# Optimization experiments

Hardware: AMD Instinct MI355X
Metric: run time of the kernel (lower is better)

## Reference

```python
import jax, jax.numpy as jnp
import numpy as np

ALPHA = 0.0  # module init alpha
BETA = 1.0   # default beta in set_target_with_data


def setup_inputs() -> dict:
    key = jax.random.key(0)
    k1, k2, k3, k4 = jax.random.split(key, 4)
    B, H, KP, N, D = 4, 16, 512, 4096, 64
    return {
        "K": jax.random.normal(k1, (B, H, KP, D), dtype=jnp.float32),
        "V": jax.random.normal(k2, (B, H, KP, D), dtype=jnp.float32),
        "xk": jax.random.normal(k3, (B, H, N, D), dtype=jnp.float32),
        "xv": jax.random.normal(k4, (B, H, N, D), dtype=jnp.float32),
    }


def reference(K, V, xk, xv):
    # set_target_with_data with dist_metric='dot', beta=1.0, beta2=None
    # dists: (B, H, k, n) = K @ xk^T
    dists = jnp.einsum('bhkd,bhnd->bhkn', K, xk)
    # softmax over the memory-slot axis (dim=-2)
    dk = jax.nn.softmax(BETA * dists, axis=-2)
    # normalize over the data axis (dim=-1)
    dkx = dk / jnp.sum(dk, axis=-1, keepdims=True)
    # weighted readout of data queries/values
    K_target = jnp.einsum('bhkn,bhnd->bhkd', dkx, xk)
    V_target = jnp.einsum('bhkn,bhnd->bhkd', dkx, xv)
    # set_target: grads used by maximize-SGD update
    gK = (1.0 - ALPHA) * (K_target - K)
    gV = (1.0 - ALPHA) * (V_target - V)
    return jnp.stack((gK, gV), axis=0)  # (2, B, H, k, d)
```

## Files before the change

### kernel.cpp

```cpp
#include <hip/hip_runtime.h>
#include <hip/hip_bf16.h>

typedef __bf16 bf16_t;
typedef __attribute__((ext_vector_type(8))) __bf16 bf16x8;
typedef __attribute__((ext_vector_type(4))) float f32x4;

#define BH 64
#define KP 512
#define NN 4096
#define DD 64
#define GSZ (BH * KP * DD)

#define MFMA16(a, b, c) __builtin_amdgcn_mfma_f32_16x16x32_bf16((a), (b), (c), 0, 0, 0)

__device__ __forceinline__ bf16x8 cvt8v(const f32x4 lo, const f32x4 hi) {
  bf16x8 r;
  r[0] = (bf16_t)lo[0]; r[1] = (bf16_t)lo[1]; r[2] = (bf16_t)lo[2]; r[3] = (bf16_t)lo[3];
  r[4] = (bf16_t)hi[0]; r[5] = (bf16_t)hi[1]; r[6] = (bf16_t)hi[2]; r[7] = (bf16_t)hi[3];
  return r;
}
__device__ __forceinline__ bf16x8 cvt8(const float* __restrict__ p) {
  return cvt8v(*(const f32x4*)p, *(const f32x4*)(p + 4));
}

__global__ __launch_bounds__(256) void hop_pass1(
    const float* __restrict__ Km, const float* __restrict__ xk,
    float* __restrict__ inv_colsum)
{
  __shared__ __align__(16) bf16_t Ks[128 * 72];

  const int tid  = threadIdx.x;
  const int wave = tid >> 6, lane = tid & 63;
  const int col  = lane & 15, quad = lane >> 4;
  const int bh = blockIdx.y;
  const int n0 = blockIdx.x * 256 + wave * 64;

  const float* Kb  = Km + (size_t)bh * KP * DD;
  const float* xkb = xk + (size_t)bh * NN * DD;

  bf16x8 bf[4][2];
  #pragma unroll
  for (int nsub = 0; nsub < 4; nsub++) {
    const float* p = xkb + (size_t)(n0 + nsub * 16 + col) * DD + quad * 8;
    bf[nsub][0] = cvt8(p);
    bf[nsub][1] = cvt8(p + 32);
  }

  float colacc[4] = {0.f, 0.f, 0.f, 0.f};
  const int srow = tid >> 1, sdo = (tid & 1) * 32;

  for (int kc = 0; kc < KP; kc += 128) {
    __syncthreads();
    const float* src = Kb + (size_t)(kc + srow) * DD + sdo;
    #pragma unroll
    for (int u = 0; u < 4; u++) {
      const f32x4 p0 = *(const f32x4*)(src + 8 * u);
      const f32x4 p1 = *(const f32x4*)(src + 8 * u + 4);
      *(bf16x8*)(Ks + srow * 72 + sdo + 8 * u) = cvt8v(p0, p1);
    }
    __syncthreads();
    #pragma unroll
    for (int ks = 0; ks < 8; ks++) {
      const bf16x8 a0 = *(const bf16x8*)(Ks + (ks * 16 + col) * 72 + quad * 8);
      const bf16x8 a1 = *(const bf16x8*)(Ks + (ks * 16 + col) * 72 + 32 + quad * 8);
      #pragma unroll
      for (int nsub = 0; nsub < 4; nsub++) {
        f32x4 c = {0.f, 0.f, 0.f, 0.f};
        c = MFMA16(a0, bf[nsub][0], c);
        c = MFMA16(a1, bf[nsub][1], c);
        colacc[nsub] += __expf(c[0]) + __expf(c[1]) + __expf(c[2]) + __expf(c[3]);
      }
    }
  }
  #pragma unroll
  for (int nsub = 0; nsub < 4; nsub++) {
    colacc[nsub] += __shfl_xor(colacc[nsub], 16, 64);
    colacc[nsub] += __shfl_xor(colacc[nsub], 32, 64);
  }
  float v = colacc[0];
  v = (quad == 1) ? colacc[1] : v;
  v = (quad == 2) ? colacc[2] : v;
  v = (quad == 3) ? colacc[3] : v;
  inv_colsum[bh * NN + n0 + quad * 16 + col] = 1.0f / v;
}

#define NT 64
#define PW 72

__global__ __launch_bounds__(256) void hop_pass2(
    const float* __restrict__ Km, const float* __restrict__ Vm,
    const float* __restrict__ xk, const float* __restrict__ xv,
    const float* __restrict__ inv_colsum, float* __restrict__ out)
{
  __shared__ __align__(16) bf16_t xks[NT * PW];
  __shared__ __align__(16) bf16_t xkT[DD * NT];
  __shared__ __align__(16) bf16_t xvT[DD * NT];
  __shared__ __align__(16) bf16_t wt[4][16 * PW];

  const int tid  = threadIdx.x;
  const int wave = tid >> 6, lane = tid & 63;
  const int col  = lane & 15, quad = lane >> 4;
  const int bh   = blockIdx.x >> 3;
  const int k0   = (blockIdx.x & 7) * 64 + wave * 16;

  const float* Kb  = Km + (size_t)bh * KP * DD;
  const float* Vb  = Vm + (size_t)bh * KP * DD;
  const float* xkb = xk + (size_t)bh * NN * DD;
  const float* xvb = xv + (size_t)bh * NN * DD;
  const float* inv = inv_colsum + bh * NN;

  const bf16x8 ak0 = cvt8(Kb + (size_t)(k0 + col) * DD + quad * 8);
  const bf16x8 ak1 = cvt8(Kb + (size_t)(k0 + col) * DD + 32 + quad * 8);

  f32x4 accK[4], accV[4];
  #pragma unroll
  for (int i = 0; i < 4; i++) {
    accK[i] = (f32x4){0.f, 0.f, 0.f, 0.f};
    accV[i] = (f32x4){0.f, 0.f, 0.f, 0.f};
  }
  float rows_part = 0.f;

  const int sn = tid >> 2;
  const int sd = (tid & 3) * 16;
  const int shi = sn >> 3, slo = sn & 7;

  for (int n0 = 0; n0 < NN; n0 += NT) {
    f32x4 gk[4], gv[4];
    #pragma unroll
    for (int u = 0; u < 4; u++) {
      gk[u] = *(const f32x4*)(xkb + (size_t)(n0 + sn) * DD + sd + 4 * u);
      gv[u] = *(const f32x4*)(xvb + (size_t)(n0 + sn) * DD + sd + 4 * u);
    }
    float ic[4];
    #pragma unroll
    for (int nsub = 0; nsub < 4; nsub++) ic[nsub] = inv[n0 + nsub * 16 + col];

    __syncthreads();

    *(bf16x8*)(xks + sn * PW + sd)     = cvt8v(gk[0], gk[1]);
    *(bf16x8*)(xks + sn * PW + sd + 8) = cvt8v(gk[2], gk[3]);
    #pragma unroll
    for (int j = 0; j < 16; j++) {
      const int d   = sd + j;
      const int off = d * NT + (((shi) ^ (d >> 3)) << 3) + slo;
      xkT[off] = (bf16_t)gk[j >> 2][j & 3];
      xvT[off] = (bf16_t)gv[j >> 2][j & 3];
    }
    __syncthreads();

    f32x4 s[4];
    #pragma unroll
    for (int nsub = 0; nsub < 4; nsub++) {
      const bf16x8 b0 = *(const bf16x8*)(xks + (nsub * 16 + col) * PW + quad * 8);
      const bf16x8 b1 = *(const bf16x8*)(xks + (nsub * 16 + col) * PW + 32 + quad * 8);
      f32x4 c = {0.f, 0.f, 0.f, 0.f};
      c = MFMA16(ak0, b0, c);
      c = MFMA16(ak1, b1, c);
      s[nsub] = c;
    }
    bf16_t* wr = wt[wave];
    #pragma unroll
    for (int nsub = 0; nsub < 4; nsub++) {
      #pragma unroll
      for (int r = 0; r < 4; r++)
        wr[(quad * 4 + r) * PW + nsub * 16 + col] = (bf16_t)(__expf(s[nsub][r]) * ic[nsub]);
    }
    const bf16x8 wa0 = *(const bf16x8*)(wr + col * PW + quad * 8);
    const bf16x8 wa1 = *(const bf16x8*)(wr + col * PW + 32 + quad * 8);
    #pragma unroll
    for (int j = 0; j < 8; j++) rows_part += (float)wa0[j] + (float)wa1[j];

    #pragma unroll
    for (int dt = 0; dt < 4; dt++) {
      const int d = dt * 16 + col, dhi = d >> 3;
      const bf16x8 bk0 = *(const bf16x8*)(xkT + d * NT + ((quad ^ dhi) << 3));
      const bf16x8 bk1 = *(const bf16x8*)(xkT + d * NT + (((4 + quad) ^ dhi) << 3));
      const bf16x8 bv0 = *(const bf16x8*)(xvT + d * NT + ((quad ^ dhi) << 3));
      const bf16x8 bv1 = *(const bf16x8*)(xvT + d * NT + (((4 + quad) ^ dhi) << 3));
      accK[dt] = MFMA16(wa0, bk0, accK[dt]);
      accK[dt] = MFMA16(wa1, bk1, accK[dt]);
      accV[dt] = MFMA16(wa0, bv0, accV[dt]);
      accV[dt] = MFMA16(wa1, bv1, accV[dt]);
    }
  }

  float rs = rows_part;
  rs += __shfl_xor(rs, 16, 64);
  rs += __shfl_xor(rs, 32, 64);
  float invrs[4];
  #pragma unroll
  for (int r = 0; r < 4; r++) invrs[r] = 1.0f / __shfl(rs, quad * 4 + r, 64);

  const size_t base = (size_t)bh * KP * DD;
  #pragma unroll
  for (int dt = 0; dt < 4; dt++) {
    #pragma unroll
    for (int r = 0; r < 4; r++) {
      const int k = k0 + quad * 4 + r;
      const int d = dt * 16 + col;
      const size_t idx = base + (size_t)k * DD + d;
      out[idx]       = accK[dt][r] * invrs[r] - Kb[(size_t)k * DD + d];
      out[GSZ + idx] = accV[dt][r] * invrs[r] - Vb[(size_t)k * DD + d];
    }
  }
}

extern "C" void kernel_launch(void* const* d_in, const int* in_sizes, int n_in,
                              void* d_out, int out_size, void* d_ws, size_t ws_size,
                              hipStream_t stream)
{
  (void)in_sizes; (void)n_in; (void)out_size; (void)ws_size;
  const float* Km = (const float*)d_in[0];
  const float* Vm = (const float*)d_in[1];
  const float* xk = (const float*)d_in[2];
  const float* xv = (const float*)d_in[3];
  float* inv_colsum = (float*)d_ws;
  float* out = (float*)d_out;

  hop_pass1<<<dim3(NN / 256, BH), 256, 0, stream>>>(Km, xk, inv_colsum);
  hop_pass2<<<BH * (KP / 64), 256, 0, stream>>>(Km, Vm, xk, xv, inv_colsum, out);
}
```

Before: 333.2 us.

## Pre-convert xk/xv to bf16 and transposed copies, double-buffer pass2 via LDS DMA

Adds a prep kernel that converts xk and xv to bf16 once per call and writes row-major and transposed copies into workspace. pass2 then stages tiles straight into LDS with global_load_lds into double buffers with XOR swizzling, which removes the per-block fp32 reload, conversion and scalar transpose. The tile for step n+1 is fetched while step n computes. The block index is also remapped to interleave bh across blocks. The cost is an extra kernel and workspace traffic, with a fallback to the old path when the workspace is too small.

```diff
diff --git a/kernel.cpp b/kernel.cpp
--- a/kernel.cpp
+++ b/kernel.cpp
@@ -23,8 +23,76 @@
   return cvt8v(*(const f32x4*)p, *(const f32x4*)(p + 4));
 }
 
+__device__ __forceinline__ void stage16(bf16_t* lds_base, const bf16_t* gsrc) {
+  __builtin_amdgcn_global_load_lds(
+      (const __attribute__((address_space(1))) void*)gsrc,
+      (__attribute__((address_space(3))) void*)lds_base, 16, 0, 0);
+}
+
+__global__ __launch_bounds__(256) void hop_prep(
+    const float* __restrict__ xk, const float* __restrict__ xv,
+    bf16_t* __restrict__ xk16, bf16_t* __restrict__ xkT16, bf16_t* __restrict__ xvT16)
+{
+  __shared__ __align__(16) bf16_t T[64 * 72];
+  const int t = threadIdx.x;
+  const int n0 = blockIdx.x * 64;
+  const int bh = blockIdx.y;
+  const int row = t >> 2;
+  const int d0  = (t & 3) * 16;
+  const int dcol = t >> 2;
+  const int nb   = (t & 3) * 16;
+  const size_t gb  = (size_t)bh * NN * DD;
+  const size_t gbT = (size_t)bh * DD * NN;
+
+  {
+    const float* src = xk + gb + (size_t)(n0 + row) * DD + d0;
+    const f32x4 a0 = *(const f32x4*)(src);
+    const f32x4 a1 = *(const f32x4*)(src + 4);
+    const f32x4 a2 = *(const f32x4*)(src + 8);
+    const f32x4 a3 = *(const f32x4*)(src + 12);
+    const bf16x8 lo = cvt8v(a0, a1), hi = cvt8v(a2, a3);
+    bf16_t* dn = xk16 + gb + (size_t)(n0 + row) * DD + d0;
+    *(bf16x8*)(dn)     = lo;
+    *(bf16x8*)(dn + 8) = hi;
+    *(bf16x8*)(T + row * 72 + d0)     = lo;
+    *(bf16x8*)(T + row * 72 + d0 + 8) = hi;
+  }
+  __syncthreads();
+  {
+    bf16x8 o0, o1;
+    #pragma unroll
+    for (int j = 0; j < 8; j++) o0[j] = T[(nb + j) * 72 + dcol];
+    #pragma unroll
+    for (int j = 0; j < 8; j++) o1[j] = T[(nb + 8 + j) * 72 + dcol];
+    bf16_t* dT = xkT16 + gbT + (size_t)dcol * NN + n0 + nb;
+    *(bf16x8*)(dT)     = o0;
+    *(bf16x8*)(dT + 8) = o1;
+  }
+  __syncthreads();
+  {
+    const float* src = xv + gb + (size_t)(n0 + row) * DD + d0;
+    const f32x4 a0 = *(const f32x4*)(src);
+    const f32x4 a1 = *(const f32x4*)(src + 4);
+    const f32x4 a2 = *(const f32x4*)(src + 8);
+    const f32x4 a3 = *(const f32x4*)(src + 12);
+    *(bf16x8*)(T + row * 72 + d0)     = cvt8v(a0, a1);
+    *(bf16x8*)(T + row * 72 + d0 + 8) = cvt8v(a2, a3);
+  }
+  __syncthreads();
+  {
+    bf16x8 o0, o1;
+    #pragma unroll
+    for (int j = 0; j < 8; j++) o0[j] = T[(nb + j) * 72 + dcol];
+    #pragma unroll
+    for (int j = 0; j < 8; j++) o1[j] = T[(nb + 8 + j) * 72 + dcol];
+    bf16_t* dT = xvT16 + gbT + (size_t)dcol * NN + n0 + nb;
+    *(bf16x8*)(dT)     = o0;
+    *(bf16x8*)(dT + 8) = o1;
+  }
+}
+
 __global__ __launch_bounds__(256) void hop_pass1(
-    const float* __restrict__ Km, const float* __restrict__ xk,
+    const float* __restrict__ Km, const bf16_t* __restrict__ xk16,
     float* __restrict__ inv_colsum)
 {
   __shared__ __align__(16) bf16_t Ks[128 * 72];
@@ -32,18 +100,19 @@
   const int tid  = threadIdx.x;
   const int wave = tid >> 6, lane = tid & 63;
   const int col  = lane & 15, quad = lane >> 4;
-  const int bh = blockIdx.y;
-  const int n0 = blockIdx.x * 256 + wave * 64;
-
-  const float* Kb  = Km + (size_t)bh * KP * DD;
-  const float* xkb = xk + (size_t)bh * NN * DD;
+  const int bid  = blockIdx.x;
+  const int bh   = (bid & 7) + 8 * ((bid >> 3) & 7);
+  const int n0   = (bid >> 6) * 256 + wave * 64;
+
+  const float*  Kb   = Km   + (size_t)bh * KP * DD;
+  const bf16_t* xkb  = xk16 + (size_t)bh * NN * DD;
 
   bf16x8 bf[4][2];
   #pragma unroll
   for (int nsub = 0; nsub < 4; nsub++) {
-    const float* p = xkb + (size_t)(n0 + nsub * 16 + col) * DD + quad * 8;
-    bf[nsub][0] = cvt8(p);
-    bf[nsub][1] = cvt8(p + 32);
+    const bf16_t* p = xkb + (size_t)(n0 + nsub * 16 + col) * DD + quad * 8;
+    bf[nsub][0] = *(const bf16x8*)(p);
+    bf[nsub][1] = *(const bf16x8*)(p + 32);
   }
 
   float colacc[4] = {0.f, 0.f, 0.f, 0.f};
@@ -89,25 +158,28 @@
 
 __global__ __launch_bounds__(256) void hop_pass2(
     const float* __restrict__ Km, const float* __restrict__ Vm,
-    const float* __restrict__ xk, const float* __restrict__ xv,
+    const bf16_t* __restrict__ xk16, const bf16_t* __restrict__ xkT16,
+    const bf16_t* __restrict__ xvT16,
     const float* __restrict__ inv_colsum, float* __restrict__ out)
 {
-  __shared__ __align__(16) bf16_t xks[NT * PW];
-  __shared__ __align__(16) bf16_t xkT[DD * NT];
-  __shared__ __align__(16) bf16_t xvT[DD * NT];
+  __shared__ __align__(16) bf16_t xks[2][NT * DD];
+  __shared__ __align__(16) bf16_t xkT[2][DD * NT];
+  __shared__ __align__(16) bf16_t xvT[2][DD * NT];
   __shared__ __align__(16) bf16_t wt[4][16 * PW];
 
   const int tid  = threadIdx.x;
   const int wave = tid >> 6, lane = tid & 63;
   const int col  = lane & 15, quad = lane >> 4;
-  const int bh   = blockIdx.x >> 3;
-  const int k0   = (blockIdx.x & 7) * 64 + wave * 16;
-
-  const float* Kb  = Km + (size_t)bh * KP * DD;
-  const float* Vb  = Vm + (size_t)bh * KP * DD;
-  const float* xkb = xk + (size_t)bh * NN * DD;
-  const float* xvb = xv + (size_t)bh * NN * DD;
-  const float* inv = inv_colsum + bh * NN;
+  const int bid  = blockIdx.x;
+  const int bh   = (bid & 7) + 8 * ((bid >> 3) & 7);
+  const int k0   = (bid >> 6) * 64 + wave * 16;
+
+  const float*  Kb   = Km    + (size_t)bh * KP * DD;
+  const float*  Vb   = Vm    + (size_t)bh * KP * DD;
+  const bf16_t* xkb  = xk16  + (size_t)bh * NN * DD;
+  const bf16_t* xkTb = xkT16 + (size_t)bh * DD * NN;
+  const bf16_t* xvTb = xvT16 + (size_t)bh * DD * NN;
+  const float*  inv  = inv_colsum + bh * NN;
 
   const bf16x8 ak0 = cvt8(Kb + (size_t)(k0 + col) * DD + quad * 8);
   const bf16x8 ak1 = cvt8(Kb + (size_t)(k0 + col) * DD + 32 + quad * 8);
@@ -120,50 +192,57 @@
   }
   float rows_part = 0.f;
 
-  const int sn = tid >> 2;
-  const int sd = (tid & 3) * 16;
-  const int shi = sn >> 3, slo = sn & 7;
-
+  const int srl = lane >> 3;
+  const int r0  = wave * 16 + srl;
+  const int r1  = r0 + 8;
+  const int sb  = ((lane & 7) ^ srl) * 8;
+  const int lb0 = (wave * 2 + 0) * 512;
+  const int lb1 = (wave * 2 + 1) * 512;
+
+  stage16(&xks[0][lb0], xkb + (size_t)r0 * DD + sb);
+  stage16(&xks[0][lb1], xkb + (size_t)r1 * DD + sb);
+  stage16(&xkT[0][lb0], xkTb + (size_t)r0 * NN + sb);
+  stage16(&xkT[0][lb1], xkTb + (size_t)r1 * NN + sb);
+  stage16(&xvT[0][lb0], xvTb + (size_t)r0 * NN + sb);
+  stage16(&xvT[0][lb1], xvTb + (size_t)r1 * NN + sb);
+  __syncthreads();
+
+  int cur = 0;
   for (int n0 = 0; n0 < NN; n0 += NT) {
-    f32x4 gk[4], gv[4];
-    #pragma unroll
-    for (int u = 0; u < 4; u++) {
-      gk[u] = *(const f32x4*)(xkb + (size_t)(n0 + sn) * DD + sd + 4 * u);
-      gv[u] = *(const f32x4*)(xvb + (size_t)(n0 + sn) * DD + sd + 4 * u);
-    }
+    if (n0 + NT < NN) {
+      const int nx = n0 + NT;
+      const int nb = cur ^ 1;
+      stage16(&xks[nb][lb0], xkb + (size_t)(nx + r0) * DD + sb);
+      stage16(&xks[nb][lb1], xkb + (size_t)(nx + r1) * DD + sb);
+      stage16(&xkT[nb][lb0], xkTb + (size_t)r0 * NN + nx + sb);
+      stage16(&xkT[nb][lb1], xkTb + (size_t)r1 * NN + nx + sb);
+      stage16(&xvT[nb][lb0], xvTb + (size_t)r0 * NN + nx + sb);
+      stage16(&xvT[nb][lb1], xvTb + (size_t)r1 * NN + nx + sb);
+    }
+
     float ic[4];
     #pragma unroll
-    for (int nsub = 0; nsub < 4; nsub++) ic[nsub] = inv[n0 + nsub * 16 + col];
-
-    __syncthreads();
-
-    *(bf16x8*)(xks + sn * PW + sd)     = cvt8v(gk[0], gk[1]);
-    *(bf16x8*)(xks + sn * PW + sd + 8) = cvt8v(gk[2], gk[3]);
-    #pragma unroll
-    for (int j = 0; j < 16; j++) {
-      const int d   = sd + j;
-      const int off = d * NT + (((shi) ^ (d >> 3)) << 3) + slo;
-      xkT[off] = (bf16_t)gk[j >> 2][j & 3];
-      xvT[off] = (bf16_t)gv[j >> 2][j & 3];
-    }
-    __syncthreads();
+    for (int ns = 0; ns < 4; ns++) ic[ns] = inv[n0 + ns * 16 + col];
+
+    const int key = col & 7;
 
     f32x4 s[4];
     #pragma unroll
-    for (int nsub = 0; nsub < 4; nsub++) {
-      const bf16x8 b0 = *(const bf16x8*)(xks + (nsub * 16 + col) * PW + quad * 8);
-      const bf16x8 b1 = *(const bf16x8*)(xks + (nsub * 16 + col) * PW + 32 + quad * 8);
+    for (int ns = 0; ns < 4; ns++) {
+      const bf16_t* bp = &xks[cur][(ns * 16 + col) * DD];
+      const bf16x8 b0 = *(const bf16x8*)(bp + 8 * (quad ^ key));
+      const bf16x8 b1 = *(const bf16x8*)(bp + 8 * ((quad + 4) ^ key));
       f32x4 c = {0.f, 0.f, 0.f, 0.f};
       c = MFMA16(ak0, b0, c);
       c = MFMA16(ak1, b1, c);
-      s[nsub] = c;
+      s[ns] = c;
     }
     bf16_t* wr = wt[wave];
     #pragma unroll
-    for (int nsub = 0; nsub < 4; nsub++) {
+    for (int ns = 0; ns < 4; ns++) {
       #pragma unroll
       for (int r = 0; r < 4; r++)
-        wr[(quad * 4 + r) * PW + nsub * 16 + col] = (bf16_t)(__expf(s[nsub][r]) * ic[nsub]);
+        wr[(quad * 4 + r) * PW + ns * 16 + col] = (bf16_t)(__expf(s[ns][r]) * ic[ns]);
     }
     const bf16x8 wa0 = *(const bf16x8*)(wr + col * PW + quad * 8);
     const bf16x8 wa1 = *(const bf16x8*)(wr + col * PW + 32 + quad * 8);
@@ -172,16 +251,21 @@
 
     #pragma unroll
     for (int dt = 0; dt < 4; dt++) {
-      const int d = dt * 16 + col, dhi = d >> 3;
-      const bf16x8 bk0 = *(const bf16x8*)(xkT + d * NT + ((quad ^ dhi) << 3));
-      const bf16x8 bk1 = *(const bf16x8*)(xkT + d * NT + (((4 + quad) ^ dhi) << 3));
-      const bf16x8 bv0 = *(const bf16x8*)(xvT + d * NT + ((quad ^ dhi) << 3));
-      const bf16x8 bv1 = *(const bf16x8*)(xvT + d * NT + (((4 + quad) ^ dhi) << 3));
+      const int d = dt * 16 + col;
+      const bf16_t* kp = &xkT[cur][d * NT];
+      const bf16_t* vp = &xvT[cur][d * NT];
+      const bf16x8 bk0 = *(const bf16x8*)(kp + 8 * (quad ^ key));
+      const bf16x8 bk1 = *(const bf16x8*)(kp + 8 * ((quad + 4) ^ key));
+      const bf16x8 bv0 = *(const bf16x8*)(vp + 8 * (quad ^ key));
+      const bf16x8 bv1 = *(const bf16x8*)(vp + 8 * ((quad + 4) ^ key));
       accK[dt] = MFMA16(wa0, bk0, accK[dt]);
       accK[dt] = MFMA16(wa1, bk1, accK[dt]);
       accV[dt] = MFMA16(wa0, bv0, accV[dt]);
       accV[dt] = MFMA16(wa1, bv1, accV[dt]);
     }
+
+    __syncthreads();
+    cur ^= 1;
   }
 
   float rs = rows_part;
@@ -205,18 +289,205 @@
   }
 }
 
+__global__ __launch_bounds__(256) void hop_pass1_fb(
+    const float* __restrict__ Km, const float* __restrict__ xk,
+    float* __restrict__ inv_colsum)
+{
+  __shared__ __align__(16) bf16_t Ks[128 * 72];
+  const int tid  = threadIdx.x;
+  const int wave = tid >> 6, lane = tid & 63;
+  const int col  = lane & 15, quad = lane >> 4;
+  const int bh = blockIdx.y;
+  const int n0 = blockIdx.x * 256 + wave * 64;
+  const float* Kb  = Km + (size_t)bh * KP * DD;
+  const float* xkb = xk + (size_t)bh * NN * DD;
+  bf16x8 bf[4][2];
+  #pragma unroll
+  for (int nsub = 0; nsub < 4; nsub++) {
+    const float* p = xkb + (size_t)(n0 + nsub * 16 + col) * DD + quad * 8;
+    bf[nsub][0] = cvt8(p);
+    bf[nsub][1] = cvt8(p + 32);
+  }
+  float colacc[4] = {0.f, 0.f, 0.f, 0.f};
+  const int srow = tid >> 1, sdo = (tid & 1) * 32;
+  for (int kc = 0; kc < KP; kc += 128) {
+    __syncthreads();
+    const float* src = Kb + (size_t)(kc + srow) * DD + sdo;
+    #pragma unroll
+    for (int u = 0; u < 4; u++) {
+      const f32x4 p0 = *(const f32x4*)(src + 8 * u);
+      const f32x4 p1 = *(const f32x4*)(src + 8 * u + 4);
+      *(bf16x8*)(Ks + srow * 72 + sdo + 8 * u) = cvt8v(p0, p1);
+    }
+    __syncthreads();
+    #pragma unroll
+    for (int ks = 0; ks < 8; ks++) {
+      const bf16x8 a0 = *(const bf16x8*)(Ks + (ks * 16 + col) * 72 + quad * 8);
+      const bf16x8 a1 = *(const bf16x8*)(Ks + (ks * 16 + col) * 72 + 32 + quad * 8);
+      #pragma unroll
+      for (int nsub = 0; nsub < 4; nsub++) {
+        f32x4 c = {0.f, 0.f, 0.f, 0.f};
+        c = MFMA16(a0, bf[nsub][0], c);
+        c = MFMA16(a1, bf[nsub][1], c);
+        colacc[nsub] += __expf(c[0]) + __expf(c[1]) + __expf(c[2]) + __expf(c[3]);
+      }
+    }
+  }
+  #pragma unroll
+  for (int nsub = 0; nsub < 4; nsub++) {
+    colacc[nsub] += __shfl_xor(colacc[nsub], 16, 64);
+    colacc[nsub] += __shfl_xor(colacc[nsub], 32, 64);
+  }
+  float v = colacc[0];
+  v = (quad == 1) ? colacc[1] : v;
+  v = (quad == 2) ? colacc[2] : v;
+  v = (quad == 3) ? colacc[3] : v;
+  inv_colsum[bh * NN + n0 + quad * 16 + col] = 1.0f / v;
+}
+
+__global__ __launch_bounds__(256) void hop_pass2_fb(
+    const float* __restrict__ Km, const float* __restrict__ Vm,
+    const float* __restrict__ xk, const float* __restrict__ xv,
+    const float* __restrict__ inv_colsum, float* __restrict__ out)
+{
+  __shared__ __align__(16) bf16_t xksf[NT * PW];
+  __shared__ __align__(16) bf16_t xkTf[DD * NT];
+  __shared__ __align__(16) bf16_t xvTf[DD * NT];
+  __shared__ __align__(16) bf16_t wtf[4][16 * PW];
+
+  const int tid  = threadIdx.x;
+  const int wave = tid >> 6, lane = tid & 63;
+  const int col  = lane & 15, quad = lane >> 4;
+  const int bh   = blockIdx.x >> 3;
+  const int k0   = (blockIdx.x & 7) * 64 + wave * 16;
+
+  const float* Kb  = Km + (size_t)bh * KP * DD;
+  const float* Vb  = Vm + (size_t)bh * KP * DD;
+  const float* xkb = xk + (size_t)bh * NN * DD;
+  const float* xvb = xv + (size_t)bh * NN * DD;
+  const float* inv = inv_colsum + bh * NN;
+
+  const bf16x8 ak0 = cvt8(Kb + (size_t)(k0 + col) * DD + quad * 8);
+  const bf16x8 ak1 = cvt8(Kb + (size_t)(k0 + col) * DD + 32 + quad * 8);
+
+  f32x4 accK[4], accV[4];
+  #pragma unroll
+  for (int i = 0; i < 4; i++) {
+    accK[i] = (f32x4){0.f, 0.f, 0.f, 0.f};
+    accV[i] = (f32x4){0.f, 0.f, 0.f, 0.f};
+  }
+  float rows_part = 0.f;
+
+  const int sn = tid >> 2;
+  const int sd = (tid & 3) * 16;
+  const int shi = sn >> 3, slo = sn & 7;
+
+  for (int n0 = 0; n0 < NN; n0 += NT) {
+    f32x4 gk[4], gv[4];
+    #pragma unroll
+    for (int u = 0; u < 4; u++) {
+      gk[u] = *(const f32x4*)(xkb + (size_t)(n0 + sn) * DD + sd + 4 * u);
+      gv[u] = *(const f32x4*)(xvb + (size_t)(n0 + sn) * DD + sd + 4 * u);
+    }
+    float ic[4];
+    #pragma unroll
+    for (int nsub = 0; nsub < 4; nsub++) ic[nsub] = inv[n0 + nsub * 16 + col];
+
+    __syncthreads();
+    *(bf16x8*)(xksf + sn * PW + sd)     = cvt8v(gk[0], gk[1]);
+    *(bf16x8*)(xksf + sn * PW + sd + 8) = cvt8v(gk[2], gk[3]);
+    #pragma unroll
+    for (int j = 0; j < 16; j++) {
+      const int d   = sd + j;
+      const int off = d * NT + (((shi) ^ (d >> 3)) << 3) + slo;
+      xkTf[off] = (bf16_t)gk[j >> 2][j & 3];
+      xvTf[off] = (bf16_t)gv[j >> 2][j & 3];
+    }
+    __syncthreads();
+
+    f32x4 s[4];
+    #pragma unroll
+    for (int nsub = 0; nsub < 4; nsub++) {
+      const bf16x8 b0 = *(const bf16x8*)(xksf + (nsub * 16 + col) * PW + quad * 8);
+      const bf16x8 b1 = *(const bf16x8*)(xksf + (nsub * 16 + col) * PW + 32 + quad * 8);
+      f32x4 c = {0.f, 0.f, 0.f, 0.f};
+      c = MFMA16(ak0, b0, c);
+      c = MFMA16(ak1, b1, c);
+      s[nsub] = c;
+    }
+    bf16_t* wr = wtf[wave];
+    #pragma unroll
+    for (int nsub = 0; nsub < 4; nsub++) {
+      #pragma unroll
+      for (int r = 0; r < 4; r++)
+        wr[(quad * 4 + r) * PW + nsub * 16 + col] = (bf16_t)(__expf(s[nsub][r]) * ic[nsub]);
+    }
+    const bf16x8 wa0 = *(const bf16x8*)(wr + col * PW + quad * 8);
+    const bf16x8 wa1 = *(const bf16x8*)(wr + col * PW + 32 + quad * 8);
+    #pragma unroll
+    for (int j = 0; j < 8; j++) rows_part += (float)wa0[j] + (float)wa1[j];
+
+    #pragma unroll
+    for (int dt = 0; dt < 4; dt++) {
+      const int d = dt * 16 + col, dhi = d >> 3;
+      const bf16x8 bk0 = *(const bf16x8*)(xkTf + d * NT + ((quad ^ dhi) << 3));
+      const bf16x8 bk1 = *(const bf16x8*)(xkTf + d * NT + (((4 + quad) ^ dhi) << 3));
+      const bf16x8 bv0 = *(const bf16x8*)(xvTf + d * NT + ((quad ^ dhi) << 3));
+      const bf16x8 bv1 = *(const bf16x8*)(xvTf + d * NT + (((4 + quad) ^ dhi) << 3));
+      accK[dt] = MFMA16(wa0, bk0, accK[dt]);
+      accK[dt] = MFMA16(wa1, bk1, accK[dt]);
+      accV[dt] = MFMA16(wa0, bv0, accV[dt]);
+      accV[dt] = MFMA16(wa1, bv1, accV[dt]);
+    }
+  }
+
+  float rs = rows_part;
+  rs += __shfl_xor(rs, 16, 64);
+  rs += __shfl_xor(rs, 32, 64);
+  float invrs[4];
+  #pragma unroll
+  for (int r = 0; r < 4; r++) invrs[r] = 1.0f / __shfl(rs, quad * 4 + r, 64);
+
+  const size_t base = (size_t)bh * KP * DD;
+  #pragma unroll
+  for (int dt = 0; dt < 4; dt++) {
+    #pragma unroll
+    for (int r = 0; r < 4; r++) {
+      const int k = k0 + quad * 4 + r;
+      const int d = dt * 16 + col;
+      const size_t idx = base + (size_t)k * DD + d;
+      out[idx]       = accK[dt][r] * invrs[r] - Kb[(size_t)k * DD + d];
+      out[GSZ + idx] = accV[dt][r] * invrs[r] - Vb[(size_t)k * DD + d];
+    }
+  }
+}
+
 extern "C" void kernel_launch(void* const* d_in, const int* in_sizes, int n_in,
                               void* d_out, int out_size, void* d_ws, size_t ws_size,
                               hipStream_t stream)
 {
-  (void)in_sizes; (void)n_in; (void)out_size; (void)ws_size;
+  (void)in_sizes; (void)n_in; (void)out_size;
   const float* Km = (const float*)d_in[0];
   const float* Vm = (const float*)d_in[1];
   const float* xk = (const float*)d_in[2];
   const float* xv = (const float*)d_in[3];
+  float* out = (float*)d_out;
   float* inv_colsum = (float*)d_ws;
-  float* out = (float*)d_out;
-
-  hop_pass1<<<dim3(NN / 256, BH), 256, 0, stream>>>(Km, xk, inv_colsum);
-  hop_pass2<<<BH * (KP / 64), 256, 0, stream>>>(Km, Vm, xk, xv, inv_colsum, out);
-}
+
+  const size_t SCRE = (size_t)BH * NN * DD;
+  const size_t NEED = (size_t)BH * NN * sizeof(float) + 3 * SCRE * sizeof(bf16_t);
+
+  if (ws_size >= NEED) {
+    bf16_t* xk16  = (bf16_t*)((char*)d_ws + (size_t)BH * NN * sizeof(float));
+    bf16_t* xkT16 = xk16 + SCRE;
+    bf16_t* xvT16 = xkT16 + SCRE;
+    hop_prep<<<dim3(NN / 64, BH), 256, 0, stream>>>(xk, xv, xk16, xkT16, xvT16);
+    hop_pass1<<<dim3((NN / 256) * BH), 256, 0, stream>>>(Km, xk16, inv_colsum);
+    hop_pass2<<<dim3(BH * (KP / 64)), 256, 0, stream>>>(Km, Vm, xk16, xkT16, xvT16,
+                                                        inv_colsum, out);
+  } else {
+    hop_pass1_fb<<<dim3(NN / 256, BH), 256, 0, stream>>>(Km, xk, inv_colsum);
+    hop_pass2_fb<<<dim3(BH * (KP / 64)), 256, 0, stream>>>(Km, Vm, xk, xv,
+                                                           inv_colsum, out);
+  }
+}
```

After: 306.4 us. 8.0% less time.
